# Kernel tuning notes

Measured on AMD Instinct MI355X. Metric: run time of the kernel, lower is better.

Reference implementation:

```python
import jax, jax.numpy as jnp
import numpy as np
from jax import lax


def _layernorm(x, g, b, eps=1e-5):
    m = x.mean(-1, keepdims=True)
    v = ((x - m) ** 2).mean(-1, keepdims=True)
    return (x - m) * lax.rsqrt(v + eps) * g + b


def _conv1d(x, w, b):
    # x: (B, T, Cin), w: (K, Cin, Cout) -> SAME padding (kernel=3, pad=1)
    y = lax.conv_general_dilated(x, w, (1,), 'SAME',
                                 dimension_numbers=('NWC', 'WIO', 'NWC'))
    return y + b


def _predictor(x, params, mask):
    w1, b1, g1, be1, w2, b2, g2, be2, wl, bl = params
    h = _layernorm(jax.nn.relu(_conv1d(x, w1, b1)), g1, be1)
    h = _layernorm(jax.nn.relu(_conv1d(h, w2, b2)), g2, be2)
    out = (h @ wl)[..., 0] + bl[0]          # (B, T)
    return jnp.where(mask, 0.0, out)


def _length_regulate(x, dur, max_len):
    # vectorized equivalent of the per-token expand/cat/pad loop
    cum = jnp.cumsum(dur, axis=1)            # (B, S)
    mel_len = cum[:, -1]                     # (B,)
    pos = jnp.arange(max_len)                # (T,)
    idx = jax.vmap(lambda c: jnp.searchsorted(c, pos, side='right'))(cum)
    idx = jnp.minimum(idx, x.shape[1] - 1)   # (B, T)
    out = jnp.take_along_axis(x, idx[:, :, None], axis=1)
    valid = (pos[None, :] < mel_len[:, None])[:, :, None]
    return jnp.where(valid, out, 0.0), mel_len


def setup_inputs() -> dict:
    key = jax.random.key(0)
    ks = jax.random.split(key, 12)
    B, S, D, F, K, T, NB = 32, 512, 512, 512, 3, 4096, 256
    inp = {
        'x': jax.random.normal(ks[0], (B, S, D), jnp.float32),
        'src_mask': jnp.zeros((B, S), bool),
        'mel_mask': jnp.zeros((B, T), bool),
        'pitch_truth': jax.random.normal(ks[1], (B, S), jnp.float32),
        'energy_truth': jax.random.normal(ks[2], (B, S), jnp.float32),
        'duration_truth': jax.random.randint(ks[3], (B, S), 0, 8, jnp.int32),
        'conv1_w': 0.05 * jax.random.normal(ks[4], (3, K, D, F), jnp.float32),
        'conv1_b': jnp.zeros((3, F), jnp.float32),
        'ln1_g': jnp.ones((3, F), jnp.float32),
        'ln1_b': jnp.zeros((3, F), jnp.float32),
        'conv2_w': 0.05 * jax.random.normal(ks[5], (3, K, F, F), jnp.float32),
        'conv2_b': jnp.zeros((3, F), jnp.float32),
        'ln2_g': jnp.ones((3, F), jnp.float32),
        'ln2_b': jnp.zeros((3, F), jnp.float32),
        'lin_w': 0.05 * jax.random.normal(ks[6], (3, F, 1), jnp.float32),
        'lin_b': jnp.zeros((3, 1), jnp.float32),
        'pitch_emb': 0.05 * jax.random.normal(ks[7], (NB, D), jnp.float32),
        'energy_emb': 0.05 * jax.random.normal(ks[8], (NB, D), jnp.float32),
        'pitch_bins': jnp.linspace(-3.0, 3.0, NB - 1),
        'energy_bins': jnp.linspace(-3.0, 3.0, NB - 1),
        'max_mel_len': T,
    }
    return inp


def reference(x, src_mask, mel_mask, pitch_truth, energy_truth, duration_truth,
              conv1_w, conv1_b, ln1_g, ln1_b, conv2_w, conv2_b, ln2_g, ln2_b,
              lin_w, lin_b, pitch_emb, energy_emb, pitch_bins, energy_bins,
              max_mel_len):
    def params(i):
        return (conv1_w[i], conv1_b[i], ln1_g[i], ln1_b[i],
                conv2_w[i], conv2_b[i], ln2_g[i], ln2_b[i], lin_w[i], lin_b[i])

    # pitch (predictor idx 0)
    pitch_pred = _predictor(x, params(0), src_mask)
    x = x + pitch_emb[jnp.searchsorted(pitch_bins, pitch_truth, side='left')]
    # energy (idx 1)
    energy_pred = _predictor(x, params(1), src_mask)
    x = x + energy_emb[jnp.searchsorted(energy_bins, energy_truth, side='left')]
    # duration (idx 2)
    log_dur = _predictor(x, params(2), src_mask)
    # length regulation with ground-truth durations (training path)
    x_out, mel_len = _length_regulate(x, duration_truth, max_mel_len)
    return x_out, pitch_pred, energy_pred, log_dur, mel_len, mel_mask
```

## Files before the change

### kernel.cpp

```cpp
#include <hip/hip_runtime.h>
#include <hip/hip_bf16.h>


#define B_ 32
#define S_ 512
#define D_ 512
#define F_ 512
#define T_ 4096
#define SP_ 514
#define KK_ 1536
#define NKT 24
#define SLOT ((size_t)B_ * SP_ * D_)

typedef __attribute__((ext_vector_type(8))) short bf16x8;
typedef __attribute__((ext_vector_type(4))) float f32x4;

__device__ __forceinline__ float bf2f(unsigned short u) {
  union { unsigned int i; float f; } c; c.i = (unsigned int)u << 16; return c.f;
}
__device__ __forceinline__ unsigned short f2bf(float f) {
  __hip_bfloat16 h = __float2bfloat16(f);
  return *(unsigned short*)&h;
}

struct Job {
  const __hip_bfloat16* Pin;
  const __hip_bfloat16* WT;
  const float* bias;
  const float* g;
  const float* be;
  const float* wl;
  const float* bl;
  const unsigned char* mask;
  __hip_bfloat16* Pout;
  float* pred;
  int mode;
};

#define WT_BLKS 1152
#define TP_BLKS 8224
__global__ __launch_bounds__(256) void prep_k(const float* __restrict__ x,
                                              const float* __restrict__ W1,
                                              const float* __restrict__ W2,
                                              const int* __restrict__ dur,
                                              const float* __restrict__ ptruth,
                                              const float* __restrict__ pbins,
                                              const float* __restrict__ pemb,
                                              const float* __restrict__ etruth,
                                              const float* __restrict__ ebins,
                                              const float* __restrict__ eemb,
                                              __hip_bfloat16* __restrict__ X0,
                                              __hip_bfloat16* __restrict__ X1,
                                              __hip_bfloat16* __restrict__ X2,
                                              __hip_bfloat16* __restrict__ P0,
                                              __hip_bfloat16* __restrict__ P1,
                                              __hip_bfloat16* __restrict__ WT1,
                                              __hip_bfloat16* __restrict__ WT2,
                                              int* __restrict__ cum,
                                              float* __restrict__ mel_len) {
  const int blk = blockIdx.x;
  const int t = threadIdx.x;
  if (blk < WT_BLKS) {
    __shared__ float tb[64][65];
    const int w = blk / 192;
    const int kt = (blk % 192) >> 3;
    const int ft = blk & 7;
    const float* src = (w < 3) ? (W1 + (size_t)w * KK_ * F_)
                               : (W2 + (size_t)(w - 3) * KK_ * F_);
    __hip_bfloat16* dst = (w < 3) ? (WT1 + (size_t)w * KK_ * F_)
                                  : (WT2 + (size_t)(w - 3) * KK_ * F_);
    const int ty = t >> 4, tx = t & 15;
    #pragma unroll
    for (int j = 0; j < 4; ++j) {
      const int r = ty + j * 16;
      const float4 v = *(const float4*)(src + (size_t)(kt * 64 + r) * F_ + ft * 64 + tx * 4);
      tb[r][tx * 4 + 0] = v.x; tb[r][tx * 4 + 1] = v.y;
      tb[r][tx * 4 + 2] = v.z; tb[r][tx * 4 + 3] = v.w;
    }
    __syncthreads();
    #pragma unroll
    for (int j = 0; j < 4; ++j) {
      const int r = ty + j * 16;
      ushort4 u = make_ushort4(f2bf(tb[tx * 4 + 0][r]), f2bf(tb[tx * 4 + 1][r]),
                               f2bf(tb[tx * 4 + 2][r]), f2bf(tb[tx * 4 + 3][r]));
      *(ushort4*)((unsigned short*)dst + (size_t)(ft * 64 + r) * KK_ + kt * 64 + tx * 4) = u;
    }
  } else if (blk < WT_BLKS + TP_BLKS) {
    __shared__ int i1s[2], i2s[2];
    const int half = t >> 7;
    const int tl = t & 127;
    const int task = (blk - WT_BLKS) * 2 + half;
    if (task < B_ * S_) {
      if (tl == 0) {
        float v = ptruth[task];
        int lo = 0, hi = 255;
        while (lo < hi) { const int mid = (lo + hi) >> 1; if (pbins[mid] < v) lo = mid + 1; else hi = mid; }
        i1s[half] = lo;
        v = etruth[task]; lo = 0; hi = 255;
        while (lo < hi) { const int mid = (lo + hi) >> 1; if (ebins[mid] < v) lo = mid + 1; else hi = mid; }
        i2s[half] = lo;
      }
      __syncthreads();
      const int b = task >> 9, s = task & 511;
      const size_t off = ((size_t)b * SP_ + s + 1) * D_ + tl * 4;
      const float4 v = *(const float4*)(x + (size_t)task * D_ + tl * 4);
      const float4 pe = *(const float4*)(pemb + (size_t)i1s[half] * D_ + tl * 4);
      const float4 ee = *(const float4*)(eemb + (size_t)i2s[half] * D_ + tl * 4);
      *(ushort4*)((unsigned short*)X0 + off) =
          make_ushort4(f2bf(v.x), f2bf(v.y), f2bf(v.z), f2bf(v.w));
      const float4 v1 = make_float4(v.x + pe.x, v.y + pe.y, v.z + pe.z, v.w + pe.w);
      *(ushort4*)((unsigned short*)X1 + off) =
          make_ushort4(f2bf(v1.x), f2bf(v1.y), f2bf(v1.z), f2bf(v1.w));
      *(ushort4*)((unsigned short*)X2 + off) =
          make_ushort4(f2bf(v1.x + ee.x), f2bf(v1.y + ee.y),
                       f2bf(v1.z + ee.z), f2bf(v1.w + ee.w));
    } else {
      __syncthreads();
      const int idx = task - B_ * S_;
      const int b = idx >> 1;
      const int r = (idx & 1) ? (SP_ - 1) : 0;
      const size_t off = ((size_t)b * SP_ + r) * D_ + tl * 4;
      const ushort4 z = make_ushort4(0, 0, 0, 0);
      *(ushort4*)((unsigned short*)X0 + off) = z;
      *(ushort4*)((unsigned short*)X1 + off) = z;
      *(ushort4*)((unsigned short*)X2 + off) = z;
      *(ushort4*)((unsigned short*)P0 + off) = z;
      *(ushort4*)((unsigned short*)P1 + off) = z;
    }
  } else {
    __shared__ int sh[S_];
    const int b = blk - (WT_BLKS + TP_BLKS);
    sh[t] = dur[b * S_ + t];
    sh[t + 256] = dur[b * S_ + t + 256];
    __syncthreads();
    for (int off = 1; off < S_; off <<= 1) {
      const int a1 = (t >= off) ? sh[t - off] : 0;
      const int j2 = t + 256;
      const int a2 = (j2 >= off) ? sh[j2 - off] : 0;
      __syncthreads();
      sh[t] += a1; sh[j2] += a2;
      __syncthreads();
    }
    cum[b * S_ + t] = sh[t];
    cum[b * S_ + t + 256] = sh[t + 256];
    if (t == 255) mel_len[b] = (float)sh[S_ - 1];
  }
}

#define GLOAD(gptr, loff) __builtin_amdgcn_global_load_lds(                    \
    (const __attribute__((address_space(1))) void*)(gptr),                     \
    (__attribute__((address_space(3))) void*)(smem + (loff)), 16, 0, 0)

__global__ __launch_bounds__(512, 2) void conv8_k(Job j0, Job j1) {
  extern __shared__ char smem[];
  const Job jb = (blockIdx.x >> 7) ? j1 : j0;
  const int inner = blockIdx.x & 127;
  const int swz = (inner & 7) * 16 + (inner >> 3);
  const int b  = swz >> 2;
  const int st = (swz & 3) * 128;
  const int t = threadIdx.x;
  const int lane = t & 63;
  const int wave = t >> 6;
  const int wm2 = wave >> 2;
  const int wn  = wave & 3;
  const int rA = lane & 15;
  const int l4 = lane >> 4;
  const int rowbase = 32 * wm2 + rA;
  const int colbase = 64 * wn + rA;

  f32x4 acc[2][2][2][4];
  #pragma unroll
  for (int a = 0; a < 2; ++a)
    #pragma unroll
    for (int c = 0; c < 2; ++c)
      #pragma unroll
      for (int m = 0; m < 2; ++m)
        #pragma unroll
        for (int n = 0; n < 4; ++n) acc[a][c][m][n] = (f32x4){0.f, 0.f, 0.f, 0.f};

  auto stageA = [&](int kt, int half) {
    const int r = t >> 3, ch = t & 7;
    const __hip_bfloat16* ga = jb.Pin +
        ((size_t)b * SP_ + st + half * 64 + r + (kt >> 3)) * D_ +
        (kt & 7) * 64 + (ch ^ (r & 7)) * 8;
    GLOAD(ga, (kt & 1) * 16384 + half * 8192 + t * 16);
  };
  auto stageB = [&](int kt, int half) {
    #pragma unroll
    for (int i = 0; i < 4; ++i) {
      const int c = t + i * 512;
      const int fr = c >> 3, ch = c & 7;
      const __hip_bfloat16* gb = jb.WT +
          (size_t)(half * 256 + fr) * KK_ + kt * 64 + (ch ^ (fr & 7)) * 8;
      GLOAD(gb, 32768 + (kt & 1) * 65536 + half * 32768 + c * 16);
    }
  };

  stageA(0, 0); stageB(0, 0); stageA(0, 1); stageB(0, 1);
  asm volatile("s_waitcnt vmcnt(0)" ::: "memory");
  __builtin_amdgcn_s_barrier();
  __builtin_amdgcn_sched_barrier(0);

  bf16x8 aA[2][2][2];
  bf16x8 bB0[2][4], bB1[2][4];

  for (int kt = 0; kt < NKT; ++kt) {
    const int cur = kt & 1;
    const char* Abase = smem + cur * 16384;
    const char* Bbase = smem + 32768 + cur * 65536;
    #pragma unroll
    for (int ah = 0; ah < 2; ++ah)
      #pragma unroll
      for (int kh = 0; kh < 2; ++kh)
        #pragma unroll
        for (int mi = 0; mi < 2; ++mi) {
          const int row = rowbase + 16 * mi;
          aA[ah][kh][mi] = *(const bf16x8*)(Abase + ah * 8192 + row * 128 +
                                            (((kh * 4 + l4) ^ (row & 7)) * 16));
        }
    #pragma unroll
    for (int kh = 0; kh < 2; ++kh)
      #pragma unroll
      for (int ni = 0; ni < 4; ++ni) {
        const int cl = colbase + 16 * ni;
        bB0[kh][ni] = *(const bf16x8*)(Bbase + cl * 128 +
                                       (((kh * 4 + l4) ^ (cl & 7)) * 16));
        bB1[kh][ni] = *(const bf16x8*)(Bbase + 32768 + cl * 128 +
                                       (((kh * 4 + l4) ^ (cl & 7)) * 16));
      }
    if (kt < NKT - 1) {
      stageA(kt + 1, 0); stageB(kt + 1, 0);
      stageA(kt + 1, 1); stageB(kt + 1, 1);
    }
    __builtin_amdgcn_s_setprio(1);
    #pragma unroll
    for (int kh = 0; kh < 2; ++kh)
      #pragma unroll
      for (int mi = 0; mi < 2; ++mi)
        #pragma unroll
        for (int ni = 0; ni < 4; ++ni)
          acc[0][0][mi][ni] = __builtin_amdgcn_mfma_f32_16x16x32_bf16(
              aA[0][kh][mi], bB0[kh][ni], acc[0][0][mi][ni], 0, 0, 0);
    #pragma unroll
    for (int kh = 0; kh < 2; ++kh)
      #pragma unroll
      for (int mi = 0; mi < 2; ++mi)
        #pragma unroll
        for (int ni = 0; ni < 4; ++ni)
          acc[1][0][mi][ni] = __builtin_amdgcn_mfma_f32_16x16x32_bf16(
              aA[1][kh][mi], bB0[kh][ni], acc[1][0][mi][ni], 0, 0, 0);
    #pragma unroll
    for (int kh = 0; kh < 2; ++kh)
      #pragma unroll
      for (int mi = 0; mi < 2; ++mi)
        #pragma unroll
        for (int ni = 0; ni < 4; ++ni)
          acc[1][1][mi][ni] = __builtin_amdgcn_mfma_f32_16x16x32_bf16(
              aA[1][kh][mi], bB1[kh][ni], acc[1][1][mi][ni], 0, 0, 0);
    #pragma unroll
    for (int kh = 0; kh < 2; ++kh)
      #pragma unroll
      for (int mi = 0; mi < 2; ++mi)
        #pragma unroll
        for (int ni = 0; ni < 4; ++ni)
          acc[0][1][mi][ni] = __builtin_amdgcn_mfma_f32_16x16x32_bf16(
              aA[0][kh][mi], bB1[kh][ni], acc[0][1][mi][ni], 0, 0, 0);
    __builtin_amdgcn_s_setprio(0);
    __builtin_amdgcn_sched_barrier(0);
    asm volatile("s_waitcnt vmcnt(0)" ::: "memory");
    __builtin_amdgcn_s_barrier();
    __builtin_amdgcn_sched_barrier(0);
  }

  float* rS = (float*)smem;
  float* rQ = rS + 512;
  float* rP = rQ + 512;
  float* tS = rP + 512;
  float* tQ = tS + 128;
  float* tP = tQ + 128;
  float* wG = tP + 128;
  float* wB = wG + 4;

  const int MODE = jb.mode;
  float bia[2][4], gg[2][4], bb[2][4], ww[2][4];
  #pragma unroll
  for (int bh = 0; bh < 2; ++bh)
    #pragma unroll
    for (int ni = 0; ni < 4; ++ni) {
      const int f = 64 * wn + bh * 256 + 16 * ni + rA;
      bia[bh][ni] = jb.bias[f]; gg[bh][ni] = jb.g[f]; bb[bh][ni] = jb.be[f];
      ww[bh][ni] = (MODE == 1) ? jb.wl[f] : 0.f;
    }
  if (MODE == 1 && wm2 == 0) {
    float gwp = 0.f, bwp = 0.f;
    #pragma unroll
    for (int bh = 0; bh < 2; ++bh)
      #pragma unroll
      for (int ni = 0; ni < 4; ++ni) {
        gwp += gg[bh][ni] * ww[bh][ni]; bwp += bb[bh][ni] * ww[bh][ni];
      }
    #pragma unroll
    for (int o = 1; o < 16; o <<= 1) {
      gwp += __shfl_xor(gwp, o); bwp += __shfl_xor(bwp, o);
    }
    if (lane == 0) { wG[wn] = gwp; wB[wn] = bwp; }
  }
  #pragma unroll
  for (int ah = 0; ah < 2; ++ah)
    #pragma unroll
    for (int mi = 0; mi < 2; ++mi)
      #pragma unroll
      for (int reg = 0; reg < 4; ++reg) {
        float sv = 0.f, sq = 0.f, sp = 0.f;
        #pragma unroll
        for (int bh = 0; bh < 2; ++bh)
          #pragma unroll
          for (int ni = 0; ni < 4; ++ni) {
            float v = fmaxf(acc[ah][bh][mi][ni][reg] + bia[bh][ni], 0.f);
            acc[ah][bh][mi][ni][reg] = v;
            sv += v; sq += v * v;
            sp += v * gg[bh][ni] * ww[bh][ni];
          }
        #pragma unroll
        for (int o = 1; o < 16; o <<= 1) {
          sv += __shfl_xor(sv, o); sq += __shfl_xor(sq, o);
          sp += __shfl_xor(sp, o);
        }
        if (rA == 0) {
          const int lr = 64 * ah + 32 * wm2 + 16 * mi + l4 * 4 + reg;
          rS[wn * 128 + lr] = sv; rQ[wn * 128 + lr] = sq; rP[wn * 128 + lr] = sp;
        }
      }
  __syncthreads();
  if (t < 128) {
    float S = 0.f, Q = 0.f, Pp = 0.f;
    #pragma unroll
    for (int w = 0; w < 4; ++w) {
      S += rS[w * 128 + t]; Q += rQ[w * 128 + t]; Pp += rP[w * 128 + t];
    }
    tS[t] = S; tQ[t] = Q; tP[t] = Pp;
  }
  __syncthreads();
  if (MODE == 0) {
    unsigned short* Pu = (unsigned short*)jb.Pout;
    #pragma unroll
    for (int ah = 0; ah < 2; ++ah)
      #pragma unroll
      for (int mi = 0; mi < 2; ++mi)
        #pragma unroll
        for (int reg = 0; reg < 4; ++reg) {
          const int lr = 64 * ah + 32 * wm2 + 16 * mi + l4 * 4 + reg;
          const float mean = tS[lr] * (1.f / F_);
          const float var = tQ[lr] * (1.f / F_) - mean * mean;
          const float inv = rsqrtf(var + 1e-5f);
          unsigned short* pp = Pu + ((size_t)b * SP_ + st + lr + 1) * D_;
          #pragma unroll
          for (int bh = 0; bh < 2; ++bh)
            #pragma unroll
            for (int ni = 0; ni < 4; ++ni)
              pp[64 * wn + bh * 256 + 16 * ni + rA] =
                  f2bf((acc[ah][bh][mi][ni][reg] - mean) * inv * gg[bh][ni] + bb[bh][ni]);
        }
  } else {
    if (t < 128) {
      const float GW = wG[0] + wG[1] + wG[2] + wG[3];
      const float BW = wB[0] + wB[1] + wB[2] + wB[3];
      const float mean = tS[t] * (1.f / F_);
      const float var = tQ[t] * (1.f / F_) - mean * mean;
      const float inv = rsqrtf(var + 1e-5f);
      const int grow = b * S_ + st + t;
      jb.pred[grow] = jb.mask[grow] ? 0.f
                                    : (inv * tP[t] - inv * mean * GW + BW + jb.bl[0]);
    }
  }
}

__global__ __launch_bounds__(256) void gather_k(const __hip_bfloat16* __restrict__ X,
                                                const int* __restrict__ cum,
                                                const unsigned char* __restrict__ melm,
                                                float* __restrict__ out,
                                                float* __restrict__ maskf) {
  const int b    = blockIdx.x >> 11;
  const int pos0 = (blockIdx.x & 2047) * 2;
  const int half = threadIdx.x >> 7;
  const int tl   = threadIdx.x & 127;
  const int pos  = pos0 + half;
  __shared__ int sidx[2], svalid[2];
  if (tl == 0) {
    const int* c = cum + b * S_;
    int lo = 0, hi = S_;
    while (lo < hi) {
      const int mid = (lo + hi) >> 1;
      if (c[mid] <= pos) lo = mid + 1; else hi = mid;
    }
    sidx[half] = (lo < S_ - 1) ? lo : (S_ - 1);
    svalid[half] = (pos < c[S_ - 1]) ? 1 : 0;
    maskf[(size_t)b * T_ + pos] = melm[(size_t)b * T_ + pos] ? 1.f : 0.f;
  }
  __syncthreads();
  float4 v = make_float4(0.f, 0.f, 0.f, 0.f);
  if (svalid[half]) {
    const ushort4 u = *(const ushort4*)((const unsigned short*)X +
                        ((size_t)b * SP_ + sidx[half] + 1) * D_ + tl * 4);
    v = make_float4(bf2f(u.x), bf2f(u.y), bf2f(u.z), bf2f(u.w));
  }
  *(float4*)(out + ((size_t)b * T_ + pos) * D_ + tl * 4) = v;
}

extern "C" void kernel_launch(void* const* d_in, const int* in_sizes, int n_in,
                              void* d_out, int out_size, void* d_ws, size_t ws_size,
                              hipStream_t stream) {
  const float* x            = (const float*)d_in[0];
  const unsigned char* srcm = (const unsigned char*)d_in[1];
  const unsigned char* melm = (const unsigned char*)d_in[2];
  const float* pitch_truth  = (const float*)d_in[3];
  const float* energy_truth = (const float*)d_in[4];
  const int*   dur          = (const int*)d_in[5];
  const float* conv1_w = (const float*)d_in[6];
  const float* conv1_b = (const float*)d_in[7];
  const float* ln1_g   = (const float*)d_in[8];
  const float* ln1_b   = (const float*)d_in[9];
  const float* conv2_w = (const float*)d_in[10];
  const float* conv2_b = (const float*)d_in[11];
  const float* ln2_g   = (const float*)d_in[12];
  const float* ln2_b   = (const float*)d_in[13];
  const float* lin_w   = (const float*)d_in[14];
  const float* lin_b   = (const float*)d_in[15];
  const float* pitch_emb   = (const float*)d_in[16];
  const float* energy_emb  = (const float*)d_in[17];
  const float* pitch_bins  = (const float*)d_in[18];
  const float* energy_bins = (const float*)d_in[19];

  float* out      = (float*)d_out;
  float* x_out    = out;
  float* p_pitch  = out + (size_t)B_ * T_ * D_;
  float* p_energy = p_pitch + B_ * S_;
  float* p_dur    = p_energy + B_ * S_;
  float* p_mellen = p_dur + B_ * S_;
  float* p_mask   = p_mellen + B_;

  __hip_bfloat16* S0  = (__hip_bfloat16*)d_ws;
  __hip_bfloat16* S1  = S0 + SLOT;
  __hip_bfloat16* S2  = S1 + SLOT;
  __hip_bfloat16* S3  = S2 + SLOT;
  __hip_bfloat16* S4  = S3 + SLOT;
  __hip_bfloat16* WT1 = S4 + SLOT;
  __hip_bfloat16* WT2 = WT1 + (size_t)3 * F_ * KK_;
  int*  cum = (int*)(WT2 + (size_t)3 * F_ * KK_);

  const dim3 blk512t(512), blk256(256);
  const int convLds = 163840;
  hipFuncSetAttribute((const void*)conv8_k,
                      hipFuncAttributeMaxDynamicSharedMemorySize, convLds);

  prep_k<<<dim3(WT_BLKS + TP_BLKS + B_), blk256, 0, stream>>>(
      x, conv1_w, conv2_w, dur, pitch_truth, pitch_bins, pitch_emb,
      energy_truth, energy_bins, energy_emb,
      S0, S1, S2, S3, S4, WT1, WT2, cum, p_mellen);

  auto c1 = [&](int i, const __hip_bfloat16* in, __hip_bfloat16* Pout) {
    return Job{in, WT1 + (size_t)i * F_ * KK_, conv1_b + (size_t)i * F_,
               ln1_g + (size_t)i * F_, ln1_b + (size_t)i * F_,
               nullptr, nullptr, nullptr, Pout, nullptr, 0};
  };
  auto c2 = [&](int i, const __hip_bfloat16* in, float* pred) {
    return Job{in, WT2 + (size_t)i * F_ * KK_, conv2_b + (size_t)i * F_,
               ln2_g + (size_t)i * F_, ln2_b + (size_t)i * F_,
               lin_w + (size_t)i * F_, lin_b + i, srcm, nullptr, pred, 1};
  };

  {
    Job a = c1(0, S0, S3), b = c1(1, S1, S4);
    conv8_k<<<dim3(256), blk512t, convLds, stream>>>(a, b);
  }
  {
    Job a = c2(0, S3, p_pitch), b = c1(2, S2, S0);
    conv8_k<<<dim3(256), blk512t, convLds, stream>>>(a, b);
  }
  {
    Job a = c2(1, S4, p_energy), b = c2(2, S0, p_dur);
    conv8_k<<<dim3(256), blk512t, convLds, stream>>>(a, b);
  }

  gather_k<<<dim3(B_ * T_ / 2), blk256, 0, stream>>>(S2, cum, melm, x_out, p_mask);
}
```

Baseline: 311.6 us.

## Load conv weights directly from global in MFMA-fragment layout, shrink LDS

```diff
diff --git a/kernel.cpp b/kernel.cpp
--- a/kernel.cpp
+++ b/kernel.cpp
@@ -10,6 +10,7 @@
 #define SP_ 514
 #define KK_ 1536
 #define NKT 24
+#define NK32 48
 #define SLOT ((size_t)B_ * SP_ * D_)
 
 typedef __attribute__((ext_vector_type(8))) short bf16x8;
@@ -67,8 +68,8 @@
     const int ft = blk & 7;
     const float* src = (w < 3) ? (W1 + (size_t)w * KK_ * F_)
                                : (W2 + (size_t)(w - 3) * KK_ * F_);
-    __hip_bfloat16* dst = (w < 3) ? (WT1 + (size_t)w * KK_ * F_)
-                                  : (WT2 + (size_t)(w - 3) * KK_ * F_);
+    __hip_bfloat16* dst = (w < 3) ? (WT1 + (size_t)w * F_ * KK_)
+                                  : (WT2 + (size_t)(w - 3) * F_ * KK_);
     const int ty = t >> 4, tx = t & 15;
     #pragma unroll
     for (int j = 0; j < 4; ++j) {
@@ -83,7 +84,12 @@
       const int r = ty + j * 16;
       ushort4 u = make_ushort4(f2bf(tb[tx * 4 + 0][r]), f2bf(tb[tx * 4 + 1][r]),
                                f2bf(tb[tx * 4 + 2][r]), f2bf(tb[tx * 4 + 3][r]));
-      *(ushort4*)((unsigned short*)dst + (size_t)(ft * 64 + r) * KK_ + kt * 64 + tx * 4) = u;
+      const int f  = ft * 64 + r;
+      const int kk = kt * 64 + tx * 4;
+      const int f16 = f >> 4, rAf = f & 15;
+      const int k32 = kk >> 5, l4v = (kk >> 3) & 3, e0 = kk & 7;
+      const size_t idx = (((size_t)(f16 * NK32 + k32)) * 64 + l4v * 16 + rAf) * 8 + e0;
+      *(ushort4*)((unsigned short*)dst + idx) = u;
     }
   } else if (blk < WT_BLKS + TP_BLKS) {
     __shared__ int i1s[2], i2s[2];
@@ -161,110 +167,63 @@
   const int t = threadIdx.x;
   const int lane = t & 63;
   const int wave = t >> 6;
-  const int wm2 = wave >> 2;
-  const int wn  = wave & 3;
   const int rA = lane & 15;
   const int l4 = lane >> 4;
-  const int rowbase = 32 * wm2 + rA;
-  const int colbase = 64 * wn + rA;
-
-  f32x4 acc[2][2][2][4];
+
+  f32x4 acc[8][4];
   #pragma unroll
-  for (int a = 0; a < 2; ++a)
-    #pragma unroll
-    for (int c = 0; c < 2; ++c)
-      #pragma unroll
-      for (int m = 0; m < 2; ++m)
-        #pragma unroll
-        for (int n = 0; n < 4; ++n) acc[a][c][m][n] = (f32x4){0.f, 0.f, 0.f, 0.f};
-
-  auto stageA = [&](int kt, int half) {
-    const int r = t >> 3, ch = t & 7;
-    const __hip_bfloat16* ga = jb.Pin +
-        ((size_t)b * SP_ + st + half * 64 + r + (kt >> 3)) * D_ +
-        (kt & 7) * 64 + (ch ^ (r & 7)) * 8;
-    GLOAD(ga, (kt & 1) * 16384 + half * 8192 + t * 16);
+  for (int m = 0; m < 8; ++m)
+    #pragma unroll
+    for (int n = 0; n < 4; ++n) acc[m][n] = (f32x4){0.f, 0.f, 0.f, 0.f};
+
+  auto stageA = [&](int kt) {
+    #pragma unroll
+    for (int i = 0; i < 2; ++i) {
+      const int c = t + i * 512;
+      const int r = c >> 3, ch = c & 7;
+      const __hip_bfloat16* ga = jb.Pin +
+          ((size_t)b * SP_ + st + r + (kt >> 3)) * D_ +
+          (kt & 7) * 64 + (ch ^ (r & 7)) * 8;
+      GLOAD(ga, (kt & 1) * 16384 + c * 16);
+    }
   };
-  auto stageB = [&](int kt, int half) {
-    #pragma unroll
-    for (int i = 0; i < 4; ++i) {
-      const int c = t + i * 512;
-      const int fr = c >> 3, ch = c & 7;
-      const __hip_bfloat16* gb = jb.WT +
-          (size_t)(half * 256 + fr) * KK_ + kt * 64 + (ch ^ (fr & 7)) * 8;
-      GLOAD(gb, 32768 + (kt & 1) * 65536 + half * 32768 + c * 16);
-    }
-  };
-
-  stageA(0, 0); stageB(0, 0); stageA(0, 1); stageB(0, 1);
+
+  const unsigned short* WTu = (const unsigned short*)jb.WT;
+
+  stageA(0);
   asm volatile("s_waitcnt vmcnt(0)" ::: "memory");
   __builtin_amdgcn_s_barrier();
   __builtin_amdgcn_sched_barrier(0);
 
-  bf16x8 aA[2][2][2];
-  bf16x8 bB0[2][4], bB1[2][4];
-
   for (int kt = 0; kt < NKT; ++kt) {
-    const int cur = kt & 1;
-    const char* Abase = smem + cur * 16384;
-    const char* Bbase = smem + 32768 + cur * 65536;
-    #pragma unroll
-    for (int ah = 0; ah < 2; ++ah)
-      #pragma unroll
-      for (int kh = 0; kh < 2; ++kh)
-        #pragma unroll
-        for (int mi = 0; mi < 2; ++mi) {
-          const int row = rowbase + 16 * mi;
-          aA[ah][kh][mi] = *(const bf16x8*)(Abase + ah * 8192 + row * 128 +
-                                            (((kh * 4 + l4) ^ (row & 7)) * 16));
-        }
+    const char* Abase = smem + (kt & 1) * 16384;
+    if (kt < NKT - 1) stageA(kt + 1);
+    bf16x8 bB[2][4];
     #pragma unroll
     for (int kh = 0; kh < 2; ++kh)
       #pragma unroll
       for (int ni = 0; ni < 4; ++ni) {
-        const int cl = colbase + 16 * ni;
-        bB0[kh][ni] = *(const bf16x8*)(Bbase + cl * 128 +
-                                       (((kh * 4 + l4) ^ (cl & 7)) * 16));
-        bB1[kh][ni] = *(const bf16x8*)(Bbase + 32768 + cl * 128 +
-                                       (((kh * 4 + l4) ^ (cl & 7)) * 16));
-      }
-    if (kt < NKT - 1) {
-      stageA(kt + 1, 0); stageB(kt + 1, 0);
-      stageA(kt + 1, 1); stageB(kt + 1, 1);
-    }
+        const size_t fidx = ((size_t)((4 * wave + ni) * NK32 + 2 * kt + kh)) * 64 + lane;
+        bB[kh][ni] = *(const bf16x8*)(WTu + fidx * 8);
+      }
+    bf16x8 aA[2][8];
+    #pragma unroll
+    for (int kh = 0; kh < 2; ++kh)
+      #pragma unroll
+      for (int mi = 0; mi < 8; ++mi) {
+        const int row = 16 * mi + rA;
+        aA[kh][mi] = *(const bf16x8*)(Abase + row * 128 +
+                                      (((kh * 4 + l4) ^ (row & 7)) * 16));
+      }
     __builtin_amdgcn_s_setprio(1);
     #pragma unroll
     for (int kh = 0; kh < 2; ++kh)
       #pragma unroll
-      for (int mi = 0; mi < 2; ++mi)
+      for (int mi = 0; mi < 8; ++mi)
         #pragma unroll
         for (int ni = 0; ni < 4; ++ni)
-          acc[0][0][mi][ni] = __builtin_amdgcn_mfma_f32_16x16x32_bf16(
-              aA[0][kh][mi], bB0[kh][ni], acc[0][0][mi][ni], 0, 0, 0);
-    #pragma unroll
-    for (int kh = 0; kh < 2; ++kh)
-      #pragma unroll
-      for (int mi = 0; mi < 2; ++mi)
-        #pragma unroll
-        for (int ni = 0; ni < 4; ++ni)
-          acc[1][0][mi][ni] = __builtin_amdgcn_mfma_f32_16x16x32_bf16(
-              aA[1][kh][mi], bB0[kh][ni], acc[1][0][mi][ni], 0, 0, 0);
-    #pragma unroll
-    for (int kh = 0; kh < 2; ++kh)
-      #pragma unroll
-      for (int mi = 0; mi < 2; ++mi)
-        #pragma unroll
-        for (int ni = 0; ni < 4; ++ni)
-          acc[1][1][mi][ni] = __builtin_amdgcn_mfma_f32_16x16x32_bf16(
-              aA[1][kh][mi], bB1[kh][ni], acc[1][1][mi][ni], 0, 0, 0);
-    #pragma unroll
-    for (int kh = 0; kh < 2; ++kh)
-      #pragma unroll
-      for (int mi = 0; mi < 2; ++mi)
-        #pragma unroll
-        for (int ni = 0; ni < 4; ++ni)
-          acc[0][1][mi][ni] = __builtin_amdgcn_mfma_f32_16x16x32_bf16(
-              aA[0][kh][mi], bB1[kh][ni], acc[0][1][mi][ni], 0, 0, 0);
+          acc[mi][ni] = __builtin_amdgcn_mfma_f32_16x16x32_bf16(
+              aA[kh][mi], bB[kh][ni], acc[mi][ni], 0, 0, 0);
     __builtin_amdgcn_s_setprio(0);
     __builtin_amdgcn_sched_barrier(0);
     asm volatile("s_waitcnt vmcnt(0)" ::: "memory");
@@ -272,70 +231,61 @@
     __builtin_amdgcn_sched_barrier(0);
   }
 
+  __syncthreads();
   float* rS = (float*)smem;
-  float* rQ = rS + 512;
-  float* rP = rQ + 512;
-  float* tS = rP + 512;
+  float* rQ = rS + 1024;
+  float* rP = rQ + 1024;
+  float* tS = rP + 1024;
   float* tQ = tS + 128;
   float* tP = tQ + 128;
   float* wG = tP + 128;
-  float* wB = wG + 4;
+  float* wB = wG + 8;
 
   const int MODE = jb.mode;
-  float bia[2][4], gg[2][4], bb[2][4], ww[2][4];
+  float bia[4], gg[4], bb[4], ww[4];
   #pragma unroll
-  for (int bh = 0; bh < 2; ++bh)
-    #pragma unroll
-    for (int ni = 0; ni < 4; ++ni) {
-      const int f = 64 * wn + bh * 256 + 16 * ni + rA;
-      bia[bh][ni] = jb.bias[f]; gg[bh][ni] = jb.g[f]; bb[bh][ni] = jb.be[f];
-      ww[bh][ni] = (MODE == 1) ? jb.wl[f] : 0.f;
-    }
-  if (MODE == 1 && wm2 == 0) {
+  for (int ni = 0; ni < 4; ++ni) {
+    const int f = 64 * wave + 16 * ni + rA;
+    bia[ni] = jb.bias[f]; gg[ni] = jb.g[f]; bb[ni] = jb.be[f];
+    ww[ni] = (MODE == 1) ? jb.wl[f] : 0.f;
+  }
+  if (MODE == 1) {
     float gwp = 0.f, bwp = 0.f;
     #pragma unroll
-    for (int bh = 0; bh < 2; ++bh)
-      #pragma unroll
-      for (int ni = 0; ni < 4; ++ni) {
-        gwp += gg[bh][ni] * ww[bh][ni]; bwp += bb[bh][ni] * ww[bh][ni];
-      }
+    for (int ni = 0; ni < 4; ++ni) { gwp += gg[ni] * ww[ni]; bwp += bb[ni] * ww[ni]; }
     #pragma unroll
     for (int o = 1; o < 16; o <<= 1) {
       gwp += __shfl_xor(gwp, o); bwp += __shfl_xor(bwp, o);
     }
-    if (lane == 0) { wG[wn] = gwp; wB[wn] = bwp; }
+    if (lane == 0) { wG[wave] = gwp; wB[wave] = bwp; }
   }
   #pragma unroll
-  for (int ah = 0; ah < 2; ++ah)
-    #pragma unroll
-    for (int mi = 0; mi < 2; ++mi)
-      #pragma unroll
-      for (int reg = 0; reg < 4; ++reg) {
-        float sv = 0.f, sq = 0.f, sp = 0.f;
-        #pragma unroll
-        for (int bh = 0; bh < 2; ++bh)
-          #pragma unroll
-          for (int ni = 0; ni < 4; ++ni) {
-            float v = fmaxf(acc[ah][bh][mi][ni][reg] + bia[bh][ni], 0.f);
-            acc[ah][bh][mi][ni][reg] = v;
-            sv += v; sq += v * v;
-            sp += v * gg[bh][ni] * ww[bh][ni];
-          }
-        #pragma unroll
-        for (int o = 1; o < 16; o <<= 1) {
-          sv += __shfl_xor(sv, o); sq += __shfl_xor(sq, o);
-          sp += __shfl_xor(sp, o);
-        }
-        if (rA == 0) {
-          const int lr = 64 * ah + 32 * wm2 + 16 * mi + l4 * 4 + reg;
-          rS[wn * 128 + lr] = sv; rQ[wn * 128 + lr] = sq; rP[wn * 128 + lr] = sp;
-        }
-      }
+  for (int mi = 0; mi < 8; ++mi)
+    #pragma unroll
+    for (int reg = 0; reg < 4; ++reg) {
+      float sv = 0.f, sq = 0.f, sp = 0.f;
+      #pragma unroll
+      for (int ni = 0; ni < 4; ++ni) {
+        float v = fmaxf(acc[mi][ni][reg] + bia[ni], 0.f);
+        acc[mi][ni][reg] = v;
+        sv += v; sq += v * v;
+        sp += v * gg[ni] * ww[ni];
+      }
+      #pragma unroll
+      for (int o = 1; o < 16; o <<= 1) {
+        sv += __shfl_xor(sv, o); sq += __shfl_xor(sq, o);
+        sp += __shfl_xor(sp, o);
+      }
+      if (rA == 0) {
+        const int lr = 16 * mi + l4 * 4 + reg;
+        rS[wave * 128 + lr] = sv; rQ[wave * 128 + lr] = sq; rP[wave * 128 + lr] = sp;
+      }
+    }
   __syncthreads();
   if (t < 128) {
     float S = 0.f, Q = 0.f, Pp = 0.f;
     #pragma unroll
-    for (int w = 0; w < 4; ++w) {
+    for (int w = 0; w < 8; ++w) {
       S += rS[w * 128 + t]; Q += rQ[w * 128 + t]; Pp += rP[w * 128 + t];
     }
     tS[t] = S; tQ[t] = Q; tP[t] = Pp;
@@ -344,27 +294,24 @@
   if (MODE == 0) {
     unsigned short* Pu = (unsigned short*)jb.Pout;
     #pragma unroll
-    for (int ah = 0; ah < 2; ++ah)
-      #pragma unroll
-      for (int mi = 0; mi < 2; ++mi)
+    for (int mi = 0; mi < 8; ++mi)
+      #pragma unroll
+      for (int reg = 0; reg < 4; ++reg) {
+        const int lr = 16 * mi + l4 * 4 + reg;
+        const float mean = tS[lr] * (1.f / F_);
+        const float var = tQ[lr] * (1.f / F_) - mean * mean;
+        const float inv = rsqrtf(var + 1e-5f);
+        unsigned short* pp = Pu + ((size_t)b * SP_ + st + lr + 1) * D_;
         #pragma unroll
-        for (int reg = 0; reg < 4; ++reg) {
-          const int lr = 64 * ah + 32 * wm2 + 16 * mi + l4 * 4 + reg;
-          const float mean = tS[lr] * (1.f / F_);
-          const float var = tQ[lr] * (1.f / F_) - mean * mean;
-          const float inv = rsqrtf(var + 1e-5f);
-          unsigned short* pp = Pu + ((size_t)b * SP_ + st + lr + 1) * D_;
-          #pragma unroll
-          for (int bh = 0; bh < 2; ++bh)
-            #pragma unroll
-            for (int ni = 0; ni < 4; ++ni)
-              pp[64 * wn + bh * 256 + 16 * ni + rA] =
-                  f2bf((acc[ah][bh][mi][ni][reg] - mean) * inv * gg[bh][ni] + bb[bh][ni]);
-        }
+        for (int ni = 0; ni < 4; ++ni)
+          pp[64 * wave + 16 * ni + rA] =
+              f2bf((acc[mi][ni][reg] - mean) * inv * gg[ni] + bb[ni]);
+      }
   } else {
     if (t < 128) {
-      const float GW = wG[0] + wG[1] + wG[2] + wG[3];
-      const float BW = wB[0] + wB[1] + wB[2] + wB[3];
+      float GW = 0.f, BW = 0.f;
+      #pragma unroll
+      for (int w = 0; w < 8; ++w) { GW += wG[w]; BW += wB[w]; }
       const float mean = tS[t] * (1.f / F_);
       const float var = tQ[t] * (1.f / F_) - mean * mean;
       const float inv = rsqrtf(var + 1e-5f);
@@ -449,7 +396,7 @@
   int*  cum = (int*)(WT2 + (size_t)3 * F_ * KK_);
 
   const dim3 blk512t(512), blk256(256);
-  const int convLds = 163840;
+  const int convLds = 49152;
   hipFuncSetAttribute((const void*)conv8_k,
                       hipFuncAttributeMaxDynamicSharedMemorySize, convLds);
 
```

Result: slower. 322.3 us (+3.4%).
